# Kernel tuning notes

Measured on AMD Instinct MI355X. Metric: run time of the kernel, lower is better.

The kernel has to match this reference:

```python
import jax, jax.numpy as jnp
import numpy as np

N_NODES = 10000
N_EDGES = 100000
DIM = 768
NEG_SLOPE = 0.2  # PyG GATConv default


def gat_conv(x, src, dst, W, att_src, att_dst, bias, num_nodes):
    """Single-head PyG-style GATConv. src/dst already include self-loops."""
    h = x @ W                                  # [N, D]
    a_s = h @ att_src                          # [N]
    a_d = h @ att_dst                          # [N]
    e = jax.nn.leaky_relu(a_s[src] + a_d[dst], NEG_SLOPE)  # [E']
    # segment softmax over edges sharing the same destination node
    m = jax.ops.segment_max(e, dst, num_segments=num_nodes)  # [N]
    e = jnp.exp(e - m[dst])
    denom = jax.ops.segment_sum(e, dst, num_segments=num_nodes)  # [N]
    alpha = e / denom[dst]                     # [E']
    msg = alpha[:, None] * h[src]              # [E', D]
    out = jax.ops.segment_sum(msg, dst, num_segments=num_nodes)  # [N, D]
    return out + bias


def setup_inputs() -> dict:
    key = jax.random.key(0)
    ks = jax.random.split(key, 12)
    s = 1.0 / np.sqrt(DIM)
    inp = {
        "x": jax.random.normal(ks[0], (N_NODES, DIM), dtype=jnp.float32),
        "edge_index": jax.random.randint(ks[1], (2, N_EDGES), 0, N_NODES, dtype=jnp.int64),
        "W1": jax.random.normal(ks[2], (DIM, DIM), dtype=jnp.float32) * s,
        "att_src1": jax.random.normal(ks[3], (DIM,), dtype=jnp.float32) * s,
        "att_dst1": jax.random.normal(ks[4], (DIM,), dtype=jnp.float32) * s,
        "b1": jnp.zeros((DIM,), dtype=jnp.float32),
        "W2": jax.random.normal(ks[5], (DIM, DIM), dtype=jnp.float32) * s,
        "att_src2": jax.random.normal(ks[6], (DIM,), dtype=jnp.float32) * s,
        "att_dst2": jax.random.normal(ks[7], (DIM,), dtype=jnp.float32) * s,
        "b2": jnp.zeros((DIM,), dtype=jnp.float32),
    }
    return inp


def reference(x, edge_index, W1, att_src1, att_dst1, b1, W2, att_src2, att_dst2, b2):
    n = x.shape[0]
    # PyG GATConv default add_self_loops=True
    loops = jnp.arange(n, dtype=edge_index.dtype)
    src = jnp.concatenate([edge_index[0], loops])
    dst = jnp.concatenate([edge_index[1], loops])
    h = gat_conv(x, src, dst, W1, att_src1, att_dst1, b1, n)
    h = jax.nn.relu(h)
    # dropout p=0.0 in eval -> identity
    out = gat_conv(h, src, dst, W2, att_src2, att_dst2, b2, n)
    return out
```

## Files before the change

### kernel.cpp

```cpp
#include <hip/hip_runtime.h>

#define DIM 768
#define NEG_SLOPE 0.2f
#define MAXDEG 64

typedef unsigned short ushort_t;
typedef short short8 __attribute__((ext_vector_type(8)));
typedef float floatx4 __attribute__((ext_vector_type(4)));

__device__ __forceinline__ ushort_t f32_to_bf16(float f) {
  unsigned int b = __float_as_uint(f);
  b += 0x7FFFu + ((b >> 16) & 1u);
  return (ushort_t)(b >> 16);
}
__device__ __forceinline__ float bf16_to_f32(ushort_t u) {
  return __uint_as_float(((unsigned int)u) << 16);
}
__device__ __forceinline__ float bf16lo(unsigned int u) {
  return __uint_as_float(u << 16);
}
__device__ __forceinline__ float bf16hi(unsigned int u) {
  return __uint_as_float(u & 0xFFFF0000u);
}
__device__ __forceinline__ unsigned int pack_bf16x2(float lo, float hi) {
  return ((unsigned int)f32_to_bf16(lo)) | (((unsigned int)f32_to_bf16(hi)) << 16);
}

__device__ __forceinline__ void gl2lds16(const ushort_t* g, ushort_t* l) {
  __builtin_amdgcn_global_load_lds(
      (const __attribute__((address_space(1))) void*)g,
      (__attribute__((address_space(3))) void*)l, 16, 0, 0);
}

__global__ __launch_bounds__(256)
void prep_kernel(const float* __restrict__ x, ushort_t* __restrict__ xb, int n4,
                 const float* __restrict__ W1, ushort_t* __restrict__ wT1,
                 const float* __restrict__ W2, ushort_t* __restrict__ wT2,
                 int* __restrict__ zbase, int nz4) {
  __shared__ ushort_t tile[64][65];
  int b = blockIdx.x;
  int t = threadIdx.x;
  if (b < 288) {
    int mat = b / 144;
    int ti = b - mat * 144;
    int tr = (ti / 12) * 64;
    int tc = (ti % 12) * 64;
    const float* W = mat ? W2 : W1;
    ushort_t* wT = mat ? wT2 : wT1;
    int lr = t >> 4, lc4 = (t & 15) * 4;
#pragma unroll
    for (int p = 0; p < 4; ++p) {
      int row = lr + p * 16;
      float4 v = *(const float4*)(W + (size_t)(tr + row) * DIM + tc + lc4);
      tile[row][lc4 + 0] = f32_to_bf16(v.x);
      tile[row][lc4 + 1] = f32_to_bf16(v.y);
      tile[row][lc4 + 2] = f32_to_bf16(v.z);
      tile[row][lc4 + 3] = f32_to_bf16(v.w);
    }
    __syncthreads();
    int n = t & 63, kb = (t >> 6) * 16;
    ushort_t tmp[16];
#pragma unroll
    for (int i = 0; i < 16; ++i) tmp[i] = tile[kb + i][n];
    ushort_t* dst = wT + (size_t)(tc + n) * DIM + tr + kb;
    *(uint4*)(dst) = *(const uint4*)(&tmp[0]);
    *(uint4*)(dst + 8) = *(const uint4*)(&tmp[8]);
  } else {
    int i = (b - 288) * 256 + t;
    if (i < n4) {
      float4 v = ((const float4*)x)[i];
      ushort4 o;
      o.x = f32_to_bf16(v.x); o.y = f32_to_bf16(v.y);
      o.z = f32_to_bf16(v.z); o.w = f32_to_bf16(v.w);
      ((ushort4*)xb)[i] = o;
    }
    if (i < nz4) {
      ((uint4*)zbase)[i] = make_uint4(0, 0, 0, 0);
    }
  }
}

__global__ void csr_kernel(const int* __restrict__ ei, int* __restrict__ deg,
                           int* __restrict__ col, int E, int Etot) {
  int e = blockIdx.x * 256 + threadIdx.x;
  if (e >= Etot) return;
  int s, d;
  if (e < E) { s = ei[e]; d = ei[E + e]; }
  else       { s = e - E; d = e - E; }
  int slot = atomicAdd(&deg[d], 1);
  if (slot < MAXDEG) col[(size_t)d * MAXDEG + slot] = s;
}

__global__ __launch_bounds__(256)
void gemm_kernel(const ushort_t* __restrict__ A, const ushort_t* __restrict__ Bt,
                 const float* __restrict__ att_s, const float* __restrict__ att_d,
                 float* __restrict__ a_s, float* __restrict__ a_d,
                 ushort_t* __restrict__ Hb, int M, int MBLK) {
  const int K = DIM;
  __shared__ __align__(16) ushort_t As[128 * 64];
  __shared__ __align__(16) ushort_t Bs[128 * 64];
  int b = blockIdx.x;
  int x = b & 7, sidx = b >> 3;
  int m_local = sidx / 6, nblk = sidx - m_local * 6;
  int mblk = x * MBLK + m_local;
  if (mblk * 128 >= M) return;
  int m0 = mblk * 128, n0 = nblk * 128;
  int tid = threadIdx.x;
  int wave = tid >> 6, lane = tid & 63;
  int quad = lane >> 4, l16 = lane & 15;
  int wr = wave >> 1, wc = wave & 1;

  floatx4 acc[4][4];
  const floatx4 fzero = {0.f, 0.f, 0.f, 0.f};
#pragma unroll
  for (int i = 0; i < 4; ++i)
#pragma unroll
    for (int j = 0; j < 4; ++j) acc[i][j] = fzero;

  int lr = lane >> 3, lc = lane & 7;
  const ushort_t* gA[4];
  const ushort_t* gB[4];
  ushort_t* lA[4];
  ushort_t* lB[4];
#pragma unroll
  for (int t = 0; t < 4; ++t) {
    int r = t * 32 + wave * 8 + lr;
    int g = lc ^ (r & 7);
    gA[t] = A + (size_t)min(m0 + r, M - 1) * K + g * 8;
    gB[t] = Bt + (size_t)(n0 + r) * K + g * 8;
    lA[t] = As + (t * 32 + wave * 8) * 64;
    lB[t] = Bs + (t * 32 + wave * 8) * 64;
  }

  for (int k0 = 0; k0 < K; k0 += 64) {
#pragma unroll
    for (int t = 0; t < 4; ++t) gl2lds16(gA[t] + k0, lA[t]);
#pragma unroll
    for (int t = 0; t < 4; ++t) gl2lds16(gB[t] + k0, lB[t]);
    __syncthreads();

#pragma unroll
    for (int h = 0; h < 2; ++h) {
      short8 af[4], bfr[4];
#pragma unroll
      for (int i = 0; i < 4; ++i) {
        int ra = wr * 64 + i * 16 + l16;
        af[i] = *(const short8*)(As + ra * 64 + ((((h << 2) | quad)) ^ (ra & 7)) * 8);
      }
#pragma unroll
      for (int j = 0; j < 4; ++j) {
        int rb = wc * 64 + j * 16 + l16;
        bfr[j] = *(const short8*)(Bs + rb * 64 + ((((h << 2) | quad)) ^ (rb & 7)) * 8);
      }
#pragma unroll
      for (int i = 0; i < 4; ++i)
#pragma unroll
        for (int j = 0; j < 4; ++j)
          acc[i][j] = __builtin_amdgcn_mfma_f32_16x16x32_bf16(af[i], bfr[j], acc[i][j], 0, 0, 0);
    }
    __syncthreads();
  }

  float avs[4], avd[4];
#pragma unroll
  for (int j = 0; j < 4; ++j) {
    int c = n0 + wc * 64 + j * 16 + l16;
    avs[j] = att_s[c];
    avd[j] = att_d[c];
  }

#pragma unroll
  for (int i = 0; i < 4; ++i) {
#pragma unroll
    for (int r2 = 0; r2 < 4; ++r2) {
      int row = m0 + wr * 64 + i * 16 + quad * 4 + r2;
      bool valid = row < M;
      float pvs = 0.f, pvd = 0.f;
#pragma unroll
      for (int j = 0; j < 4; ++j) {
        float v = acc[i][j][r2];
        if (valid) Hb[(size_t)row * DIM + n0 + wc * 64 + j * 16 + l16] = f32_to_bf16(v);
        pvs = fmaf(v, avs[j], pvs);
        pvd = fmaf(v, avd[j], pvd);
      }
#pragma unroll
      for (int off = 1; off < 16; off <<= 1) {
        pvs += __shfl_xor(pvs, off, 64);
        pvd += __shfl_xor(pvd, off, 64);
      }
      if (valid && l16 == 0) {
        atomicAdd(a_s + row, pvs);
        atomicAdd(a_d + row, pvd);
      }
    }
  }
}

__global__ __launch_bounds__(256)
void aggregate_kernel(const ushort_t* __restrict__ h, const float* __restrict__ a_s,
                      const float* __restrict__ a_d, const int* __restrict__ deg,
                      const int* __restrict__ col, const float* __restrict__ bias,
                      float* __restrict__ out_f32, ushort_t* __restrict__ out_bf16,
                      int relu_mode, int N) {
  int wave = threadIdx.x >> 6, lane = threadIdx.x & 63;
  int node = blockIdx.x * 4 + wave;
  if (node >= N) return;
  int dg = min(deg[node], MAXDEG);
  int start = node * MAXDEG, end = start + dg;
  float ad = a_d[node];

  float vmax = -3.4e38f;
  for (int e = start + lane; e < end; e += 64) {
    float v = a_s[col[e]] + ad;
    v = (v > 0.f) ? v : NEG_SLOPE * v;
    vmax = fmaxf(vmax, v);
  }
#pragma unroll
  for (int off = 32; off > 0; off >>= 1) vmax = fmaxf(vmax, __shfl_xor(vmax, off, 64));

  float ssum = 0.f;
  for (int e = start + lane; e < end; e += 64) {
    float v = a_s[col[e]] + ad;
    v = (v > 0.f) ? v : NEG_SLOPE * v;
    ssum += __expf(v - vmax);
  }
#pragma unroll
  for (int off = 32; off > 0; off >>= 1) ssum += __shfl_xor(ssum, off, 64);
  float inv = 1.f / ssum;

  float acc8[8];
  float acc4[4];
#pragma unroll
  for (int k = 0; k < 8; ++k) acc8[k] = 0.f;
#pragma unroll
  for (int k = 0; k < 4; ++k) acc4[k] = 0.f;

  for (int base = start; base < end; base += 64) {
    int e = base + lane;
    float al = 0.f;
    int sc = 0;
    if (e < end) {
      sc = col[e];
      float v = a_s[sc] + ad;
      v = (v > 0.f) ? v : NEG_SLOPE * v;
      al = __expf(v - vmax) * inv;
    }
    int cnt = min(64, end - base);
    float w = __shfl(al, 0, 64);
    int s = __shfl(sc, 0, 64);
    const ushort_t* hr = h + (size_t)s * DIM;
    uint4 u = *(const uint4*)(hr + lane * 8);
    ushort4 t4 = *(const ushort4*)(hr + 512 + lane * 4);
    for (int j = 0; j < cnt; ++j) {
      float wn_ = 0.f;
      uint4 un;
      ushort4 tn;
      if (j + 1 < cnt) {
        wn_ = __shfl(al, j + 1, 64);
        int sn = __shfl(sc, j + 1, 64);
        const ushort_t* hrn = h + (size_t)sn * DIM;
        un = *(const uint4*)(hrn + lane * 8);
        tn = *(const ushort4*)(hrn + 512 + lane * 4);
      }
      acc8[0] = fmaf(w, bf16lo(u.x), acc8[0]);
      acc8[1] = fmaf(w, bf16hi(u.x), acc8[1]);
      acc8[2] = fmaf(w, bf16lo(u.y), acc8[2]);
      acc8[3] = fmaf(w, bf16hi(u.y), acc8[3]);
      acc8[4] = fmaf(w, bf16lo(u.z), acc8[4]);
      acc8[5] = fmaf(w, bf16hi(u.z), acc8[5]);
      acc8[6] = fmaf(w, bf16lo(u.w), acc8[6]);
      acc8[7] = fmaf(w, bf16hi(u.w), acc8[7]);
      acc4[0] = fmaf(w, bf16_to_f32(t4.x), acc4[0]);
      acc4[1] = fmaf(w, bf16_to_f32(t4.y), acc4[1]);
      acc4[2] = fmaf(w, bf16_to_f32(t4.z), acc4[2]);
      acc4[3] = fmaf(w, bf16_to_f32(t4.w), acc4[3]);
      if (j + 1 < cnt) { w = wn_; u = un; t4 = tn; }
    }
  }

  size_t ob = (size_t)node * DIM;
  int c8 = lane * 8, c4 = 512 + lane * 4;
  float4 b0 = *(const float4*)(bias + c8);
  float4 b1 = *(const float4*)(bias + c8 + 4);
  float4 b2 = *(const float4*)(bias + c4);
  float o[12];
  o[0] = acc8[0] + b0.x; o[1] = acc8[1] + b0.y;
  o[2] = acc8[2] + b0.z; o[3] = acc8[3] + b0.w;
  o[4] = acc8[4] + b1.x; o[5] = acc8[5] + b1.y;
  o[6] = acc8[6] + b1.z; o[7] = acc8[7] + b1.w;
  o[8] = acc4[0] + b2.x; o[9] = acc4[1] + b2.y;
  o[10] = acc4[2] + b2.z; o[11] = acc4[3] + b2.w;
  if (relu_mode) {
#pragma unroll
    for (int k = 0; k < 12; ++k) o[k] = fmaxf(o[k], 0.f);
    uint4 s0;
    s0.x = pack_bf16x2(o[0], o[1]);
    s0.y = pack_bf16x2(o[2], o[3]);
    s0.z = pack_bf16x2(o[4], o[5]);
    s0.w = pack_bf16x2(o[6], o[7]);
    *(uint4*)(out_bf16 + ob + c8) = s0;
    uint2 s1;
    s1.x = pack_bf16x2(o[8], o[9]);
    s1.y = pack_bf16x2(o[10], o[11]);
    *(uint2*)(out_bf16 + ob + c4) = s1;
  } else {
    *(float4*)(out_f32 + ob + c8) = make_float4(o[0], o[1], o[2], o[3]);
    *(float4*)(out_f32 + ob + c8 + 4) = make_float4(o[4], o[5], o[6], o[7]);
    *(float4*)(out_f32 + ob + c4) = make_float4(o[8], o[9], o[10], o[11]);
  }
}

extern "C" void kernel_launch(void* const* d_in, const int* in_sizes, int n_in,
                              void* d_out, int out_size, void* d_ws, size_t ws_size,
                              hipStream_t stream) {
  const float* x   = (const float*)d_in[0];
  const int*   ei  = (const int*)d_in[1];
  const float* W1  = (const float*)d_in[2];
  const float* as1 = (const float*)d_in[3];
  const float* ad1 = (const float*)d_in[4];
  const float* b1  = (const float*)d_in[5];
  const float* W2  = (const float*)d_in[6];
  const float* as2 = (const float*)d_in[7];
  const float* ad2 = (const float*)d_in[8];
  const float* b2  = (const float*)d_in[9];

  const int N = in_sizes[0] / DIM;
  const int E = in_sizes[1] / 2;
  const int Etot = E + N;

  char* p = (char*)d_ws;
  auto alloc = [&](size_t bytes) {
    char* q = p;
    p += (bytes + 255) & ~(size_t)255;
    return q;
  };
  ushort_t* Hb     = (ushort_t*)alloc((size_t)N * DIM * 2);
  ushort_t* xb     = (ushort_t*)alloc((size_t)N * DIM * 2);
  ushort_t* wT1    = (ushort_t*)alloc((size_t)DIM * DIM * 2);
  ushort_t* wT2    = (ushort_t*)alloc((size_t)DIM * DIM * 2);
  int*      zbase  = (int*)alloc((size_t)5 * N * 4 + 16);
  int*      deg    = zbase;
  float*    a_s1   = (float*)(zbase + N);
  float*    a_d1   = (float*)(zbase + 2 * N);
  float*    a_s2   = (float*)(zbase + 3 * N);
  float*    a_d2   = (float*)(zbase + 4 * N);
  int*      col    = (int*)alloc((size_t)N * MAXDEG * 4);

  int n4 = N * DIM / 4;
  int nz4 = (5 * N + 3) / 4;
  int prep_blocks = 288 + (n4 + 255) / 256;
  prep_kernel<<<prep_blocks, 256, 0, stream>>>(x, xb, n4, W1, wT1, W2, wT2,
                                               zbase, nz4);
  csr_kernel<<<(Etot + 255) / 256, 256, 0, stream>>>(ei, deg, col, E, Etot);

  int MB = (N + 127) / 128;
  int MBLK = (MB + 7) / 8;
  int gemm_blocks = 8 * MBLK * 6;
  int agg_blocks = (N + 3) / 4;

  gemm_kernel<<<gemm_blocks, 256, 0, stream>>>(xb, wT1, as1, ad1, a_s1, a_d1, Hb, N, MBLK);
  aggregate_kernel<<<agg_blocks, 256, 0, stream>>>(Hb, a_s1, a_d1, deg, col, b1,
                                                   nullptr, xb, 1, N);
  gemm_kernel<<<gemm_blocks, 256, 0, stream>>>(xb, wT2, as2, ad2, a_s2, a_d2, Hb, N, MBLK);
  aggregate_kernel<<<agg_blocks, 256, 0, stream>>>(Hb, a_s2, a_d2, deg, col, b2,
                                                   (float*)d_out, nullptr, 0, N);
}
```

Measured before the change: 208.0 us.

## Double-buffer GEMM LDS tiles and batch neighbor gathers in aggregation

The GEMM now uses two LDS buffers, so the global-to-LDS copy of the next K tile is issued before the MFMAs on the current tile, with one barrier per iteration instead of two. The aggregation kernel computes each edge's attention logit once per lane, relying on degree being capped at 64 so a single wave covers every edge, and reuses that value for both the softmax max and the sum. It then gathers neighbor rows in groups of four using two ping-pong register sets to keep more loads in flight. The cost is double the LDS per block, which can lower occupancy, and higher register pressure. Padded slots past the real degree load a clamped valid column with zero weight.

```diff
diff --git a/kernel.cpp b/kernel.cpp
--- a/kernel.cpp
+++ b/kernel.cpp
@@ -97,8 +97,8 @@
                  float* __restrict__ a_s, float* __restrict__ a_d,
                  ushort_t* __restrict__ Hb, int M, int MBLK) {
   const int K = DIM;
-  __shared__ __align__(16) ushort_t As[128 * 64];
-  __shared__ __align__(16) ushort_t Bs[128 * 64];
+  __shared__ __align__(16) ushort_t As[2][128 * 64];
+  __shared__ __align__(16) ushort_t Bs[2][128 * 64];
   int b = blockIdx.x;
   int x = b & 7, sidx = b >> 3;
   int m_local = sidx / 6, nblk = sidx - m_local * 6;
@@ -128,29 +128,38 @@
     int g = lc ^ (r & 7);
     gA[t] = A + (size_t)min(m0 + r, M - 1) * K + g * 8;
     gB[t] = Bt + (size_t)(n0 + r) * K + g * 8;
-    lA[t] = As + (t * 32 + wave * 8) * 64;
-    lB[t] = Bs + (t * 32 + wave * 8) * 64;
-  }
+    lA[t] = &As[0][(t * 32 + wave * 8) * 64];
+    lB[t] = &Bs[0][(t * 32 + wave * 8) * 64];
+  }
+
+#define GEMM_STAGE(k0_, buf_)                                         \
+  {                                                                   \
+    _Pragma("unroll")                                                 \
+    for (int t = 0; t < 4; ++t) gl2lds16(gA[t] + (k0_), lA[t] + (buf_)*8192); \
+    _Pragma("unroll")                                                 \
+    for (int t = 0; t < 4; ++t) gl2lds16(gB[t] + (k0_), lB[t] + (buf_)*8192); \
+  }
+
+  GEMM_STAGE(0, 0);
+  __syncthreads();
+  int cur = 0;
 
   for (int k0 = 0; k0 < K; k0 += 64) {
-#pragma unroll
-    for (int t = 0; t < 4; ++t) gl2lds16(gA[t] + k0, lA[t]);
-#pragma unroll
-    for (int t = 0; t < 4; ++t) gl2lds16(gB[t] + k0, lB[t]);
-    __syncthreads();
-
+    if (k0 + 64 < K) GEMM_STAGE(k0 + 64, cur ^ 1);
+    const ushort_t* Ab = &As[cur][0];
+    const ushort_t* Bb = &Bs[cur][0];
 #pragma unroll
     for (int h = 0; h < 2; ++h) {
       short8 af[4], bfr[4];
 #pragma unroll
       for (int i = 0; i < 4; ++i) {
         int ra = wr * 64 + i * 16 + l16;
-        af[i] = *(const short8*)(As + ra * 64 + ((((h << 2) | quad)) ^ (ra & 7)) * 8);
+        af[i] = *(const short8*)(Ab + ra * 64 + ((((h << 2) | quad)) ^ (ra & 7)) * 8);
       }
 #pragma unroll
       for (int j = 0; j < 4; ++j) {
         int rb = wc * 64 + j * 16 + l16;
-        bfr[j] = *(const short8*)(Bs + rb * 64 + ((((h << 2) | quad)) ^ (rb & 7)) * 8);
+        bfr[j] = *(const short8*)(Bb + rb * 64 + ((((h << 2) | quad)) ^ (rb & 7)) * 8);
       }
 #pragma unroll
       for (int i = 0; i < 4; ++i)
@@ -159,6 +168,7 @@
           acc[i][j] = __builtin_amdgcn_mfma_f32_16x16x32_bf16(af[i], bfr[j], acc[i][j], 0, 0, 0);
     }
     __syncthreads();
+    cur ^= 1;
   }
 
   float avs[4], avd[4];
@@ -206,27 +216,21 @@
   int node = blockIdx.x * 4 + wave;
   if (node >= N) return;
   int dg = min(deg[node], MAXDEG);
-  int start = node * MAXDEG, end = start + dg;
+  int base = node * MAXDEG;
   float ad = a_d[node];
 
-  float vmax = -3.4e38f;
-  for (int e = start + lane; e < end; e += 64) {
-    float v = a_s[col[e]] + ad;
-    v = (v > 0.f) ? v : NEG_SLOPE * v;
-    vmax = fmaxf(vmax, v);
-  }
+  bool has = lane < dg;
+  int sc = col[base + min(lane, dg - 1)];
+  float v = a_s[sc] + ad;
+  v = (v > 0.f) ? v : NEG_SLOPE * v;
+  float vmax = v;
 #pragma unroll
   for (int off = 32; off > 0; off >>= 1) vmax = fmaxf(vmax, __shfl_xor(vmax, off, 64));
-
-  float ssum = 0.f;
-  for (int e = start + lane; e < end; e += 64) {
-    float v = a_s[col[e]] + ad;
-    v = (v > 0.f) ? v : NEG_SLOPE * v;
-    ssum += __expf(v - vmax);
-  }
+  float ex = has ? __expf(v - vmax) : 0.f;
+  float ssum = ex;
 #pragma unroll
   for (int off = 32; off > 0; off >>= 1) ssum += __shfl_xor(ssum, off, 64);
-  float inv = 1.f / ssum;
+  float al = ex * (1.f / ssum);
 
   float acc8[8];
   float acc4[4];
@@ -235,47 +239,50 @@
 #pragma unroll
   for (int k = 0; k < 4; ++k) acc4[k] = 0.f;
 
-  for (int base = start; base < end; base += 64) {
-    int e = base + lane;
-    float al = 0.f;
-    int sc = 0;
-    if (e < end) {
-      sc = col[e];
-      float v = a_s[sc] + ad;
-      v = (v > 0.f) ? v : NEG_SLOPE * v;
-      al = __expf(v - vmax) * inv;
-    }
-    int cnt = min(64, end - base);
-    float w = __shfl(al, 0, 64);
-    int s = __shfl(sc, 0, 64);
-    const ushort_t* hr = h + (size_t)s * DIM;
-    uint4 u = *(const uint4*)(hr + lane * 8);
-    ushort4 t4 = *(const ushort4*)(hr + 512 + lane * 4);
-    for (int j = 0; j < cnt; ++j) {
-      float wn_ = 0.f;
-      uint4 un;
-      ushort4 tn;
-      if (j + 1 < cnt) {
-        wn_ = __shfl(al, j + 1, 64);
-        int sn = __shfl(sc, j + 1, 64);
-        const ushort_t* hrn = h + (size_t)sn * DIM;
-        un = *(const uint4*)(hrn + lane * 8);
-        tn = *(const ushort4*)(hrn + 512 + lane * 4);
-      }
-      acc8[0] = fmaf(w, bf16lo(u.x), acc8[0]);
-      acc8[1] = fmaf(w, bf16hi(u.x), acc8[1]);
-      acc8[2] = fmaf(w, bf16lo(u.y), acc8[2]);
-      acc8[3] = fmaf(w, bf16hi(u.y), acc8[3]);
-      acc8[4] = fmaf(w, bf16lo(u.z), acc8[4]);
-      acc8[5] = fmaf(w, bf16hi(u.z), acc8[5]);
-      acc8[6] = fmaf(w, bf16lo(u.w), acc8[6]);
-      acc8[7] = fmaf(w, bf16hi(u.w), acc8[7]);
-      acc4[0] = fmaf(w, bf16_to_f32(t4.x), acc4[0]);
-      acc4[1] = fmaf(w, bf16_to_f32(t4.y), acc4[1]);
-      acc4[2] = fmaf(w, bf16_to_f32(t4.z), acc4[2]);
-      acc4[3] = fmaf(w, bf16_to_f32(t4.w), acc4[3]);
-      if (j + 1 < cnt) { w = wn_; u = un; t4 = tn; }
-    }
+  uint4 uA[4], uB[4];
+  ushort4 tA[4], tB[4];
+  float wA[4], wB[4];
+
+#define GAT_LOADC(b_, u_, t_, w_)                                     \
+  {                                                                   \
+    _Pragma("unroll")                                                 \
+    for (int q = 0; q < 4; ++q) {                                     \
+      int j_ = (b_) + q;                                              \
+      w_[q] = __shfl(al, j_, 64);                                     \
+      int s_ = __shfl(sc, j_, 64);                                    \
+      const ushort_t* hr_ = h + (size_t)s_ * DIM;                     \
+      u_[q] = *(const uint4*)(hr_ + lane * 8);                        \
+      t_[q] = *(const ushort4*)(hr_ + 512 + lane * 4);                \
+    }                                                                 \
+  }
+
+#define GAT_FMAC(u_, t_, w_)                                          \
+  {                                                                   \
+    _Pragma("unroll")                                                 \
+    for (int q = 0; q < 4; ++q) {                                     \
+      float w = w_[q];                                                \
+      acc8[0] = fmaf(w, bf16lo(u_[q].x), acc8[0]);                    \
+      acc8[1] = fmaf(w, bf16hi(u_[q].x), acc8[1]);                    \
+      acc8[2] = fmaf(w, bf16lo(u_[q].y), acc8[2]);                    \
+      acc8[3] = fmaf(w, bf16hi(u_[q].y), acc8[3]);                    \
+      acc8[4] = fmaf(w, bf16lo(u_[q].z), acc8[4]);                    \
+      acc8[5] = fmaf(w, bf16hi(u_[q].z), acc8[5]);                    \
+      acc8[6] = fmaf(w, bf16lo(u_[q].w), acc8[6]);                    \
+      acc8[7] = fmaf(w, bf16hi(u_[q].w), acc8[7]);                    \
+      acc4[0] = fmaf(w, bf16_to_f32(t_[q].x), acc4[0]);               \
+      acc4[1] = fmaf(w, bf16_to_f32(t_[q].y), acc4[1]);               \
+      acc4[2] = fmaf(w, bf16_to_f32(t_[q].z), acc4[2]);               \
+      acc4[3] = fmaf(w, bf16_to_f32(t_[q].w), acc4[3]);               \
+    }                                                                 \
+  }
+
+  int dgc = (dg + 3) & ~3;
+  GAT_LOADC(0, uA, tA, wA);
+  for (int b = 0; b < dgc; b += 8) {
+    if (b + 4 < dgc) GAT_LOADC(b + 4, uB, tB, wB);
+    GAT_FMAC(uA, tA, wA);
+    if (b + 8 < dgc) GAT_LOADC(b + 8, uA, tA, wA);
+    if (b + 4 < dgc) GAT_FMAC(uB, tB, wB);
   }
 
   size_t ob = (size_t)node * DIM;
```

Result: faster. 200.5 us (-3.6%).
